# Optimization experiments

Measured on AMD Instinct MI355X. Metric: run time of the kernel, lower is better.

## Reference

```python
import jax, jax.numpy as jnp
import numpy as np

ALPHA = 0.8
TOPK = 9
LOW_BOUND = 0.0
EPS = 1e-10
IOU_EPS = 1e-6


def pairwise_iou(boxes1, boxes2):
    # boxes1 [N,4], boxes2 [G,4] in x1,y1,x2,y2 -> IoU [N,G] (mmdet BboxOverlaps2D)
    area1 = (boxes1[:, 2] - boxes1[:, 0]) * (boxes1[:, 3] - boxes1[:, 1])  # [N]
    area2 = (boxes2[:, 2] - boxes2[:, 0]) * (boxes2[:, 3] - boxes2[:, 1])  # [G]
    lt = jnp.maximum(boxes1[:, None, :2], boxes2[None, :, :2])  # [N,G,2]
    rb = jnp.minimum(boxes1[:, None, 2:], boxes2[None, :, 2:])  # [N,G,2]
    wh = jnp.clip(rb - lt, 0.0)
    inter = wh[..., 0] * wh[..., 1]  # [N,G]
    union = area1[:, None] + area2[None, :] - inter
    return inter / jnp.maximum(union, IOU_EPS)


def setup_inputs() -> dict:
    key = jax.random.key(0)
    k1, k2, k3, k4, k5, k6, k7 = jax.random.split(key, 7)
    N, G, C = 65536, 256, 80
    IMG = 1024.0
    points = jax.random.uniform(k1, (N, 2), dtype=jnp.float32) * IMG  # (cy, cx)
    p_xy1 = jax.random.uniform(k2, (N, 2), dtype=jnp.float32) * (IMG - 96.0)
    p_wh = jax.random.uniform(k3, (N, 2), dtype=jnp.float32) * 95.0 + 1.0
    bbox_preds = jnp.concatenate([p_xy1, p_xy1 + p_wh], axis=1)  # valid x1y1x2y2
    g_xy1 = jax.random.uniform(k4, (G, 2), dtype=jnp.float32) * (IMG - 256.0)
    g_wh = jax.random.uniform(k5, (G, 2), dtype=jnp.float32) * 255.0 + 1.0
    gt_bboxes = jnp.concatenate([g_xy1, g_xy1 + g_wh], axis=1)
    cls_scores = jax.random.normal(k6, (N, C), dtype=jnp.float32)
    gt_labels = jax.random.randint(k7, (G,), 0, C)
    return {"points": points, "cls_scores": cls_scores, "bbox_preds": bbox_preds,
            "gt_bboxes": gt_bboxes, "gt_labels": gt_labels}


def reference(points, cls_scores, bbox_preds, gt_bboxes, gt_labels):
    num_points = points.shape[0]
    num_gt = gt_bboxes.shape[0]
    overlaps = pairwise_iou(bbox_preds, gt_bboxes)  # [N,G]
    cls_cost = jax.nn.sigmoid(cls_scores[:, gt_labels])  # [N,G]
    overlaps = cls_cost ** (1.0 - ALPHA) * overlaps ** ALPHA
    # top-k points per GT (torch: overlaps.topk(k, dim=0))
    _, topk_idxs = jax.lax.top_k(overlaps.T, TOPK)  # [G,K]
    candidate_idxs = topk_idxs.T  # [K,G]
    cp = jnp.transpose(points[candidate_idxs], (1, 0, 2))  # [G,K,2] (cy,cx)
    # mle_2d_gaussian_2: per-GT MLE Gaussian over candidate points
    miu = cp.mean(axis=1, keepdims=True)  # [G,1,2]
    diff = cp - miu  # [G,K,2]
    sigma = jnp.einsum('gki,gkj->gij', diff, diff) / TOPK  # [G,2,2]
    a, b = sigma[:, 0, 0], sigma[:, 0, 1]
    c, d = sigma[:, 1, 0], sigma[:, 1, 1]
    det = a * d - b * c  # [G]
    inv = jnp.stack([jnp.stack([d, -b], axis=-1),
                     jnp.stack([-c, a], axis=-1)], axis=-2) / (det + EPS)[:, None, None]
    maha = jnp.einsum('gki,gij,gkj->gk', diff, inv, diff)  # [G,K]
    candidate_w = jnp.exp(-0.5 * maha).T  # [K,G]
    # center-inside-gt validity, evaluated only at candidate points
    cy, cx = cp[:, :, 0], cp[:, :, 1]  # [G,K]
    gx1, gy1, gx2, gy2 = (gt_bboxes[:, i][:, None] for i in range(4))  # [G,1]
    valid = ((cx - gx1 > EPS) & (cy - gy1 > EPS) &
             (gx2 - cx > EPS) & (gy2 - cy > EPS)).T  # [K,G]
    wv = candidate_w * valid.astype(candidate_w.dtype)
    # scatter per-GT weights to points, then max over GTs == scatter-max
    w = jnp.zeros((num_points,), dtype=cls_scores.dtype)
    w = w.at[candidate_idxs.reshape(-1)].max(wv.reshape(-1))
    w = jnp.where(w < LOW_BOUND, jnp.zeros_like(w), w)
    return w
```

## Files before the change

kernel.cpp:

```cpp
#include <hip/hip_runtime.h>
#include <hip/hip_bf16.h>
#include <math.h>

#define NPTS   65536
#define NGT    256
#define NCLS   80
#define TOPK   9
#define GSLICE 32
#define NPB    256
#define SCAP   64

__device__ inline unsigned long long pack_key(float L, unsigned idx) {
    unsigned u   = __float_as_uint(L);
    unsigned k32 = (u & 0x80000000u) ? ~u : (u | 0x80000000u);
    return ((unsigned long long)k32 << 32) | (unsigned)(~idx);
}

__global__ void zero_cnt_kernel(unsigned* __restrict__ cnt) {
    cnt[threadIdx.x] = 0u;
}

__global__ __launch_bounds__(256) void filter_kernel(
    const float* __restrict__ preds,
    const float* __restrict__ gtb,
    unsigned*    __restrict__ cnt,
    unsigned long long* __restrict__ bucket,
    int cap,
    float* __restrict__ w)
{
    __shared__ float4   gbox[GSLICE];
    __shared__ unsigned lcnt[GSLICE];
    __shared__ unsigned gbase[GSLICE];
    __shared__ unsigned long long stage[GSLICE][SCAP];

    const int t   = threadIdx.x;
    const int pt  = blockIdx.x * NPB + t;
    const int g0  = blockIdx.y * GSLICE;
    const int bid = blockIdx.y * (NPTS / NPB) + blockIdx.x;

    if (t < GSLICE) {
        gbox[t] = ((const float4*)gtb)[g0 + t];
        lcnt[t] = 0u;
    }
    if (t < NPTS / (NPB / GSLICE * (NGT / GSLICE) * (NPTS / NPB) / (NPTS / NPB)) / 2048 + 32) {  }
    if (t < 32) w[bid * 32 + t] = 0.0f;

    float4 pb = ((const float4*)preds)[pt];
    float parea = (pb.z - pb.x) * (pb.w - pb.y);
    __syncthreads();

    for (int gi = 0; gi < GSLICE; ++gi) {
        float4 g4 = gbox[gi];
        float ix1 = fmaxf(pb.x, g4.x), iy1 = fmaxf(pb.y, g4.y);
        float ix2 = fminf(pb.z, g4.z), iy2 = fminf(pb.w, g4.w);
        float iw  = fmaxf(ix2 - ix1, 0.0f);
        float ih  = fmaxf(iy2 - iy1, 0.0f);
        float inter = iw * ih;
        if (inter > 0.0f) {
            float garea = (g4.z - g4.x) * (g4.w - g4.y);
            float uni = fmaxf(parea + garea - inter, 1e-6f);
            float iou = inter / uni;
            unsigned long long entry =
                ((unsigned long long)__float_as_uint(iou) << 32) |
                (unsigned)(~(unsigned)pt);
            unsigned slot = atomicAdd(&lcnt[gi], 1u);
            if (slot < SCAP) {
                stage[gi][slot] = entry;
            } else {
                unsigned pos = atomicAdd(&cnt[g0 + gi], 1u);
                if (pos < (unsigned)cap)
                    bucket[(size_t)(g0 + gi) * cap + pos] = entry;
            }
        }
    }
    __syncthreads();

    if (t < GSLICE) {
        unsigned c = lcnt[t];
        if (c > SCAP) c = SCAP;
        lcnt[t]  = c;
        gbase[t] = atomicAdd(&cnt[g0 + t], c);
    }
    __syncthreads();

    for (int i = t; i < GSLICE * SCAP; i += 256) {
        int gi = i >> 6;
        int sl = i & (SCAP - 1);
        if (sl < (int)lcnt[gi]) {
            unsigned pos = gbase[gi] + (unsigned)sl;
            if (pos < (unsigned)cap)
                bucket[(size_t)(g0 + gi) * cap + pos] = stage[gi][sl];
        }
    }
}

__global__ __launch_bounds__(256) void select_kernel(
    const unsigned*           __restrict__ cnt,
    const unsigned long long* __restrict__ bucket,
    const float* __restrict__ cls,
    const int*   __restrict__ glab,
    const float* __restrict__ pts,
    const float* __restrict__ gtb,
    float* __restrict__ w,
    int cap)
{
    const int g    = blockIdx.x;
    const int t    = threadIdx.x;
    const int lane = t & 63;
    const int wid  = t >> 6;

    __shared__ unsigned long long wl[4][TOPK];
    __shared__ unsigned tidx[TOPK];
    __shared__ float ppy[TOPK], ppx[TOPK];

    int n = (int)cnt[g];
    if (n > cap) n = cap;
    const int lab = glab[g];
    const float E1 = 1.0f - 0.8f;

    unsigned long long loc[TOPK];
#pragma unroll
    for (int k = 0; k < TOPK; ++k) loc[k] = 0ULL;
    if (t < TOPK) loc[0] = pack_key(-INFINITY, (unsigned)t);

    const unsigned long long* src = bucket + (size_t)g * cap;

    int i = t;
    for (; i + 3 * 256 < n; i += 4 * 256) {
        unsigned long long v[4];
        float x[4];
#pragma unroll
        for (int j = 0; j < 4; ++j) v[j] = src[i + j * 256];
#pragma unroll
        for (int j = 0; j < 4; ++j) {
            unsigned p = ~(unsigned)(v[j] & 0xFFFFFFFFu);
            x[j] = cls[(size_t)p * NCLS + lab];
        }
#pragma unroll
        for (int j = 0; j < 4; ++j) {
            float iou = __uint_as_float((unsigned)(v[j] >> 32));
            float s   = 1.0f / (1.0f + expf(-x[j]));
            float L   = E1 * log2f(s) + 0.8f * log2f(iou);
            unsigned u   = __float_as_uint(L);
            unsigned k32 = (u & 0x80000000u) ? ~u : (u | 0x80000000u);
            unsigned long long key =
                ((unsigned long long)k32 << 32) | (v[j] & 0xFFFFFFFFu);
            if (key > loc[TOPK - 1]) {
                loc[TOPK - 1] = key;
#pragma unroll
                for (int jj = TOPK - 1; jj > 0; --jj)
                    if (loc[jj] > loc[jj - 1]) {
                        unsigned long long tmp = loc[jj];
                        loc[jj] = loc[jj - 1]; loc[jj - 1] = tmp;
                    }
            }
        }
    }
    for (; i < n; i += 256) {
        unsigned long long v = src[i];
        unsigned p = ~(unsigned)(v & 0xFFFFFFFFu);
        float x   = cls[(size_t)p * NCLS + lab];
        float iou = __uint_as_float((unsigned)(v >> 32));
        float s   = 1.0f / (1.0f + expf(-x));
        float L   = E1 * log2f(s) + 0.8f * log2f(iou);
        unsigned u   = __float_as_uint(L);
        unsigned k32 = (u & 0x80000000u) ? ~u : (u | 0x80000000u);
        unsigned long long key =
            ((unsigned long long)k32 << 32) | (v & 0xFFFFFFFFu);
        if (key > loc[TOPK - 1]) {
            loc[TOPK - 1] = key;
#pragma unroll
            for (int jj = TOPK - 1; jj > 0; --jj)
                if (loc[jj] > loc[jj - 1]) {
                    unsigned long long tmp = loc[jj];
                    loc[jj] = loc[jj - 1]; loc[jj - 1] = tmp;
                }
        }
    }
#pragma unroll
    for (int a = 0; a < TOPK; ++a)
#pragma unroll
        for (int j = TOPK - 1; j > 0; --j)
            if (loc[j] > loc[j - 1]) {
                unsigned long long tmp = loc[j];
                loc[j] = loc[j - 1]; loc[j - 1] = tmp;
            }

#pragma unroll
    for (int lvl = 0; lvl < 6; ++lvl) {
        const int off = 1 << lvl;
        unsigned long long oth[TOPK];
#pragma unroll
        for (int k = 0; k < TOPK; ++k) oth[k] = __shfl_xor(loc[k], off);
#pragma unroll
        for (int k = 0; k < TOPK; ++k) {
            unsigned long long v = oth[k];
            if (v > loc[TOPK - 1]) {
                loc[TOPK - 1] = v;
#pragma unroll
                for (int j = TOPK - 1; j > 0; --j) {
                    if (loc[j] > loc[j - 1]) {
                        unsigned long long tmp = loc[j];
                        loc[j] = loc[j - 1]; loc[j - 1] = tmp;
                    }
                }
            }
        }
    }

    if (lane == 0) {
#pragma unroll
        for (int k = 0; k < TOPK; ++k) wl[wid][k] = loc[k];
    }
    __syncthreads();

    if (t == 0) {
#pragma unroll
        for (int wv = 1; wv < 4; ++wv) {
#pragma unroll
            for (int k = 0; k < TOPK; ++k) {
                unsigned long long v = wl[wv][k];
                if (v > loc[TOPK - 1]) {
                    loc[TOPK - 1] = v;
#pragma unroll
                    for (int j = TOPK - 1; j > 0; --j) {
                        if (loc[j] > loc[j - 1]) {
                            unsigned long long tmp = loc[j];
                            loc[j] = loc[j - 1]; loc[j - 1] = tmp;
                        }
                    }
                }
            }
        }
#pragma unroll
        for (int k = 0; k < TOPK; ++k)
            tidx[k] = ~(unsigned)(loc[k] & 0xFFFFFFFFu);
    }
    __syncthreads();

    if (t < TOPK) {
        unsigned pi = tidx[t];
        ppy[t] = pts[2 * (size_t)pi];
        ppx[t] = pts[2 * (size_t)pi + 1];
    }
    __syncthreads();

    if (t == 0) {
        float4 g4 = ((const float4*)gtb)[g];
        float m0 = 0.0f, m1 = 0.0f;
#pragma unroll
        for (int k = 0; k < TOPK; ++k) { m0 += ppy[k]; m1 += ppx[k]; }
        m0 /= (float)TOPK; m1 /= (float)TOPK;

        float d0[TOPK], d1[TOPK];
        float a = 0.0f, bb = 0.0f, dd = 0.0f;
#pragma unroll
        for (int k = 0; k < TOPK; ++k) {
            d0[k] = ppy[k] - m0;
            d1[k] = ppx[k] - m1;
            a  += d0[k] * d0[k];
            bb += d0[k] * d1[k];
            dd += d1[k] * d1[k];
        }
        a /= (float)TOPK; bb /= (float)TOPK; dd /= (float)TOPK;
        float det  = a * dd - bb * bb;
        float rinv = 1.0f / (det + 1e-10f);

#pragma unroll
        for (int k = 0; k < TOPK; ++k) {
            float q = d0[k] * (dd * d0[k] - bb * d1[k])
                    + d1[k] * (a  * d1[k] - bb * d0[k]);
            float maha = q * rinv;
            float wt = expf(-0.5f * maha);
            bool valid = (ppx[k] - g4.x > 1e-10f) && (ppy[k] - g4.y > 1e-10f) &&
                         (g4.z - ppx[k] > 1e-10f) && (g4.w - ppy[k] > 1e-10f);
            float wv = valid ? wt : 0.0f;
            atomicMax((int*)&w[tidx[k]], __float_as_int(wv));
        }
    }
}

extern "C" void kernel_launch(void* const* d_in, const int* in_sizes, int n_in,
                              void* d_out, int out_size, void* d_ws, size_t ws_size,
                              hipStream_t stream) {
    const float* points  = (const float*)d_in[0];
    const float* cls     = (const float*)d_in[1];
    const float* preds   = (const float*)d_in[2];
    const float* gtb     = (const float*)d_in[3];
    const int*   glab    = (const int*)d_in[4];
    float* w = (float*)d_out;

    unsigned*           cnt    = (unsigned*)d_ws;
    unsigned long long* bucket = (unsigned long long*)((char*)d_ws + 1024);

    long long avail = ((long long)ws_size - 1024) / (NGT * (long long)sizeof(unsigned long long));
    int cap = (avail < 8192) ? (int)avail : 8192;

    zero_cnt_kernel<<<1, NGT, 0, stream>>>(cnt);
    filter_kernel<<<dim3(NPTS / NPB, NGT / GSLICE), 256, 0, stream>>>(
        preds, gtb, cnt, bucket, cap, w);
    select_kernel<<<NGT, 256, 0, stream>>>(cnt, bucket, cls, glab, points, gtb, w, cap);
}
```

Baseline: 129.4 us.

## Replace global atomic candidate buckets with fixed per-block slots and drop zero kernel

The global per-GT atomic counter and compacted bucket are replaced by a fixed slot per (GT, point-block) pair of size SCAP, with a per-slot count array. The zero-count kernel launch and the global atomics go away, and in select each thread scans one block's slot. GT boxes are now read from global memory instead of shared memory. The risks are load imbalance across threads in select, a larger workspace footprint, and silently dropping candidates when a block has more than SCAP hits for one GT.

New measurement: 139.7 us. 8.0% more time.

```diff
diff --git a/kernel.cpp b/kernel.cpp
--- a/kernel.cpp
+++ b/kernel.cpp
@@ -8,6 +8,7 @@
 #define TOPK   9
 #define GSLICE 32
 #define NPB    256
+#define NXB    (NPTS / NPB)
 #define SCAP   64
 
 __device__ inline unsigned long long pack_key(float L, unsigned idx) {
@@ -16,33 +17,23 @@
     return ((unsigned long long)k32 << 32) | (unsigned)(~idx);
 }
 
-__global__ void zero_cnt_kernel(unsigned* __restrict__ cnt) {
-    cnt[threadIdx.x] = 0u;
-}
-
 __global__ __launch_bounds__(256) void filter_kernel(
     const float* __restrict__ preds,
     const float* __restrict__ gtb,
-    unsigned*    __restrict__ cnt,
+    unsigned short* __restrict__ counts,
     unsigned long long* __restrict__ bucket,
-    int cap,
     float* __restrict__ w)
 {
-    __shared__ float4   gbox[GSLICE];
     __shared__ unsigned lcnt[GSLICE];
-    __shared__ unsigned gbase[GSLICE];
     __shared__ unsigned long long stage[GSLICE][SCAP];
 
     const int t   = threadIdx.x;
-    const int pt  = blockIdx.x * NPB + t;
+    const int xb  = blockIdx.x;
     const int g0  = blockIdx.y * GSLICE;
-    const int bid = blockIdx.y * (NPTS / NPB) + blockIdx.x;
-
-    if (t < GSLICE) {
-        gbox[t] = ((const float4*)gtb)[g0 + t];
-        lcnt[t] = 0u;
-    }
-    if (t < NPTS / (NPB / GSLICE * (NGT / GSLICE) * (NPTS / NPB) / (NPTS / NPB)) / 2048 + 32) {  }
+    const int pt  = xb * NPB + t;
+    const int bid = blockIdx.y * NXB + xb;
+
+    if (t < GSLICE) lcnt[t] = 0u;
     if (t < 32) w[bid * 32 + t] = 0.0f;
 
     float4 pb = ((const float4*)preds)[pt];
@@ -50,7 +41,7 @@
     __syncthreads();
 
     for (int gi = 0; gi < GSLICE; ++gi) {
-        float4 g4 = gbox[gi];
+        const float4 g4 = ((const float4*)gtb)[g0 + gi];
         float ix1 = fmaxf(pb.x, g4.x), iy1 = fmaxf(pb.y, g4.y);
         float ix2 = fminf(pb.z, g4.z), iy2 = fminf(pb.w, g4.w);
         float iw  = fmaxf(ix2 - ix1, 0.0f);
@@ -64,13 +55,7 @@
                 ((unsigned long long)__float_as_uint(iou) << 32) |
                 (unsigned)(~(unsigned)pt);
             unsigned slot = atomicAdd(&lcnt[gi], 1u);
-            if (slot < SCAP) {
-                stage[gi][slot] = entry;
-            } else {
-                unsigned pos = atomicAdd(&cnt[g0 + gi], 1u);
-                if (pos < (unsigned)cap)
-                    bucket[(size_t)(g0 + gi) * cap + pos] = entry;
-            }
+            if (slot < SCAP) stage[gi][slot] = entry;
         }
     }
     __syncthreads();
@@ -78,31 +63,27 @@
     if (t < GSLICE) {
         unsigned c = lcnt[t];
         if (c > SCAP) c = SCAP;
-        lcnt[t]  = c;
-        gbase[t] = atomicAdd(&cnt[g0 + t], c);
+        lcnt[t] = c;
+        counts[(size_t)(g0 + t) * NXB + xb] = (unsigned short)c;
     }
     __syncthreads();
 
     for (int i = t; i < GSLICE * SCAP; i += 256) {
         int gi = i >> 6;
         int sl = i & (SCAP - 1);
-        if (sl < (int)lcnt[gi]) {
-            unsigned pos = gbase[gi] + (unsigned)sl;
-            if (pos < (unsigned)cap)
-                bucket[(size_t)(g0 + gi) * cap + pos] = stage[gi][sl];
-        }
+        if (sl < (int)lcnt[gi])
+            bucket[((size_t)(g0 + gi) * NXB + xb) * SCAP + sl] = stage[gi][sl];
     }
 }
 
 __global__ __launch_bounds__(256) void select_kernel(
-    const unsigned*           __restrict__ cnt,
+    const unsigned short*     __restrict__ counts,
     const unsigned long long* __restrict__ bucket,
     const float* __restrict__ cls,
     const int*   __restrict__ glab,
     const float* __restrict__ pts,
     const float* __restrict__ gtb,
-    float* __restrict__ w,
-    int cap)
+    float* __restrict__ w)
 {
     const int g    = blockIdx.x;
     const int t    = threadIdx.x;
@@ -113,8 +94,6 @@
     __shared__ unsigned tidx[TOPK];
     __shared__ float ppy[TOPK], ppx[TOPK];
 
-    int n = (int)cnt[g];
-    if (n > cap) n = cap;
     const int lab = glab[g];
     const float E1 = 1.0f - 0.8f;
 
@@ -123,41 +102,10 @@
     for (int k = 0; k < TOPK; ++k) loc[k] = 0ULL;
     if (t < TOPK) loc[0] = pack_key(-INFINITY, (unsigned)t);
 
-    const unsigned long long* src = bucket + (size_t)g * cap;
-
-    int i = t;
-    for (; i + 3 * 256 < n; i += 4 * 256) {
-        unsigned long long v[4];
-        float x[4];
-#pragma unroll
-        for (int j = 0; j < 4; ++j) v[j] = src[i + j * 256];
-#pragma unroll
-        for (int j = 0; j < 4; ++j) {
-            unsigned p = ~(unsigned)(v[j] & 0xFFFFFFFFu);
-            x[j] = cls[(size_t)p * NCLS + lab];
-        }
-#pragma unroll
-        for (int j = 0; j < 4; ++j) {
-            float iou = __uint_as_float((unsigned)(v[j] >> 32));
-            float s   = 1.0f / (1.0f + expf(-x[j]));
-            float L   = E1 * log2f(s) + 0.8f * log2f(iou);
-            unsigned u   = __float_as_uint(L);
-            unsigned k32 = (u & 0x80000000u) ? ~u : (u | 0x80000000u);
-            unsigned long long key =
-                ((unsigned long long)k32 << 32) | (v[j] & 0xFFFFFFFFu);
-            if (key > loc[TOPK - 1]) {
-                loc[TOPK - 1] = key;
-#pragma unroll
-                for (int jj = TOPK - 1; jj > 0; --jj)
-                    if (loc[jj] > loc[jj - 1]) {
-                        unsigned long long tmp = loc[jj];
-                        loc[jj] = loc[jj - 1]; loc[jj - 1] = tmp;
-                    }
-            }
-        }
-    }
-    for (; i < n; i += 256) {
-        unsigned long long v = src[i];
+    int c = (int)counts[(size_t)g * NXB + t];
+    const unsigned long long* src = bucket + ((size_t)g * NXB + t) * SCAP;
+    for (int j = 0; j < c; ++j) {
+        unsigned long long v = src[j];
         unsigned p = ~(unsigned)(v & 0xFFFFFFFFu);
         float x   = cls[(size_t)p * NCLS + lab];
         float iou = __uint_as_float((unsigned)(v >> 32));
@@ -290,14 +238,12 @@
     const int*   glab    = (const int*)d_in[4];
     float* w = (float*)d_out;
 
-    unsigned*           cnt    = (unsigned*)d_ws;
-    unsigned long long* bucket = (unsigned long long*)((char*)d_ws + 1024);
-
-    long long avail = ((long long)ws_size - 1024) / (NGT * (long long)sizeof(unsigned long long));
-    int cap = (avail < 8192) ? (int)avail : 8192;
-
-    zero_cnt_kernel<<<1, NGT, 0, stream>>>(cnt);
-    filter_kernel<<<dim3(NPTS / NPB, NGT / GSLICE), 256, 0, stream>>>(
-        preds, gtb, cnt, bucket, cap, w);
-    select_kernel<<<NGT, 256, 0, stream>>>(cnt, bucket, cls, glab, points, gtb, w, cap);
-}
+    unsigned long long* bucket = (unsigned long long*)d_ws;
+    unsigned short* counts =
+        (unsigned short*)((char*)d_ws + (size_t)NGT * NXB * SCAP * 8);
+
+    filter_kernel<<<dim3(NXB, NGT / GSLICE), 256, 0, stream>>>(
+        preds, gtb, counts, bucket, w);
+    select_kernel<<<NGT, 256, 0, stream>>>(
+        counts, bucket, cls, glab, points, gtb, w);
+}
```
